# Kernel tuning notes

Measured on AMD Instinct MI355X. Metric: run time of the kernel, lower is better.

## Reference

```python
import jax, jax.numpy as jnp
import numpy as np


def setup_inputs() -> dict:
    key = jax.random.key(0)
    k1, k2, k3, k4, k5, k6 = jax.random.split(key, 6)
    B, V = 128, 128000
    logits = jax.random.normal(k1, (B, V), dtype=jnp.float32) * 2.0
    # keep temperatures away from 0 to avoid overflow in logits/temp
    temperatures = 0.7 + 0.6 * jax.random.uniform(k2, (B,), dtype=jnp.float32)
    top_ks = jax.random.randint(k3, (B,), 1, 1024, dtype=jnp.int32)
    top_ps = 0.7 + 0.29 * jax.random.uniform(k4, (B,), dtype=jnp.float32)
    min_ps = 0.02 * jax.random.uniform(k5, (B,), dtype=jnp.float32)
    # uniform variate for inverse-CDF multinomial sampling (one sample per row)
    u = jax.random.uniform(k6, (B, 1), dtype=jnp.float32)
    return {
        "logits": logits,
        "temperatures": temperatures,
        "top_ks": top_ks,
        "top_ps": top_ps,
        "min_ps": min_ps,
        "u": u,
    }


def reference(logits, temperatures, top_ks, top_ps, min_ps, u):
    """Faithful jax version of Sampler's torch-native sampling path:
    softmax(logits/T) -> descending sort -> top-k mask -> top-p mask
    (cumsum computed pre-mask, exactly as torch code) -> min-p mask ->
    multinomial sample (inverse CDF with provided uniform u) ->
    gather original token index. Also returns the renormalized filtered
    probs scattered back to vocab order (top_p_normalize_probs-style)."""
    B, V = logits.shape
    probs = jax.nn.softmax(logits / temperatures[:, None], axis=-1)  # [B, V]

    order = jnp.argsort(-probs, axis=-1)                     # descending indices
    probs_sort = jnp.take_along_axis(probs, order, axis=-1)  # [B, V] sorted desc
    probs_sum = jnp.cumsum(probs_sort, axis=-1)              # cumsum BEFORE masking

    pos = jnp.arange(V, dtype=jnp.int32)[None, :]
    # top-k: zero everything at rank >= top_k
    probs_sort = jnp.where(pos >= top_ks[:, None], 0.0, probs_sort)
    # top-p: zero where cumulative mass strictly before this token exceeds top_p
    probs_sort = jnp.where(probs_sum - probs_sort > top_ps[:, None], 0.0, probs_sort)
    # min-p: threshold relative to the max prob (rank-0 entry survives both masks)
    min_p_thr = probs_sort[:, :1] * min_ps[:, None]
    probs_sort = jnp.where(probs_sort < min_p_thr, 0.0, probs_sort)

    total = jnp.sum(probs_sort, axis=-1, keepdims=True)      # [B, 1]
    cdf = jnp.cumsum(probs_sort, axis=-1) / total            # normalized CDF
    # inverse-CDF sampling == torch.multinomial(probs_sort, 1)
    sampled_rank = jnp.clip(jnp.sum(cdf < u, axis=-1, keepdims=True), 0, V - 1)
    token_ids = jnp.take_along_axis(order, sampled_rank, axis=-1)[:, 0].astype(jnp.int32)

    # scatter renormalized filtered probs back to original vocab positions
    inv_order = jnp.argsort(order, axis=-1)
    norm_probs = jnp.take_along_axis(probs_sort / total, inv_order, axis=-1)
    return token_ids, norm_probs
```

## Files before the change

### kernel.cpp

```cpp
#include <hip/hip_runtime.h>
#include <stdint.h>
#include <math.h>

#define TPB 1024
#define NB 2048
#define SPLIT 4
#define LCAND 2560
#define CAND2 2048
#define PS 4096
#define L2E 1.44269504088896f

typedef float vfloat4 __attribute__((ext_vector_type(4)));
typedef unsigned long long ull;

__device__ __forceinline__ unsigned fkey(float f) {
    unsigned u = __float_as_uint(f);
    return (u & 0x80000000u) ? ~u : (u | 0x80000000u);
}
__device__ __forceinline__ float funkey(unsigned k) {
    unsigned u = (k & 0x80000000u) ? (k ^ 0x80000000u) : ~k;
    return __uint_as_float(u);
}
__device__ __forceinline__ ull packkv(unsigned k, unsigned idx) {
    return ((ull)k << 32) | (ull)(~idx);
}

__device__ __forceinline__ float inv_norm_tail(float p) {
    float t = sqrtf(-2.0f * logf(p));
    float num = 2.515517f + t * (0.802853f + t * 0.010328f);
    float den = 1.0f + t * (1.432788f + t * (0.189269f + t * 0.001308f));
    return t - num / den;
}

__device__ __forceinline__ void suffix_scan_2048(unsigned* h, unsigned* wscr, int tid)
{
    const int lane = tid & 63, w = tid >> 6;
    const int i0 = 2047 - 2 * tid;
    const int i1 = 2046 - 2 * tid;
    unsigned a = h[i0], b = h[i1];
    unsigned s = a + b;
    unsigned inc = s;
    #pragma unroll
    for (int d = 1; d < 64; d <<= 1) { unsigned o = __shfl_up(inc, d); if (lane >= d) inc += o; }
    if (lane == 63) wscr[w] = inc;
    __syncthreads();
    if (w == 0) {
        unsigned v = (lane < 16) ? wscr[lane] : 0u;
        unsigned vi = v;
        #pragma unroll
        for (int d = 1; d < 16; d <<= 1) { unsigned o = __shfl_up(vi, d); if (lane >= d) vi += o; }
        if (lane < 16) wscr[16 + lane] = vi - v;
    }
    __syncthreads();
    unsigned off = wscr[16 + w] + (inc - s);
    h[i0] = off + a;
    h[i1] = off + a + b;
    __syncthreads();
}

__global__ __launch_bounds__(TPB)
void k1_scan(const float* __restrict__ logits,
             const float* __restrict__ temps,
             const int* __restrict__ top_ks,
             float* __restrict__ out_probs,
             float* __restrict__ ws_meta,
             unsigned* __restrict__ ws_cut,
             unsigned* __restrict__ ws_cnt,
             unsigned* __restrict__ ws_max,
             ull* __restrict__ ws_cand,
             int V, int Vq)
{
    const int sblk = blockIdx.x;
    const int b = sblk / SPLIT, s = sblk % SPLIT;
    const int tid = threadIdx.x, lane = tid & 63, w = tid >> 6;
    const int start = s * Vq;
    const int len = min(Vq, V - start);
    const int slot = sblk;
    const float invT = 1.0f / temps[b];
    int K = top_ks[b]; K = max(K, 1); K = min(K, 1024);

    __shared__ float fred[52];
    __shared__ unsigned uscr[32];
    __shared__ unsigned cnt;

    if (len <= 0) {
        if (tid == 0) {
            ws_meta[2*slot] = -1e30f; ws_meta[2*slot+1] = 0.0f;
            ws_cut[slot] = 0xFFFFFFFFu; ws_cnt[slot] = 0u; ws_max[slot] = 0u;
        }
        return;
    }

    if (tid == 0) cnt = 0;

    const float* __restrict__ row = logits + (size_t)b * V + start;
    const vfloat4* __restrict__ row4 = (const vfloat4*)row;
    float* __restrict__ orow = out_probs + (size_t)b * V + start;
    vfloat4* __restrict__ orow4 = (vfloat4*)orow;
    const vfloat4 z4 = (vfloat4)0.0f;
    const int L4 = len >> 2;
    const bool vec = (len >= 4 * TPB);
    const int nps = vec ? (4 * TPB) : min(len, PS);

    float sm = 0.0f, sq = 0.0f, m0 = -1e30f;
    vfloat4 pv = z4;
    if (vec) {
        pv = row4[tid];
        __builtin_nontemporal_store(z4, &orow4[tid]);
        sm = (pv[0] + pv[1]) + (pv[2] + pv[3]);
        sq = (pv[0]*pv[0] + pv[1]*pv[1]) + (pv[2]*pv[2] + pv[3]*pv[3]);
        m0 = fmaxf(fmaxf(pv[0], pv[1]), fmaxf(pv[2], pv[3]));
    } else {
        for (int i = tid; i < nps; i += TPB) {
            float lv = row[i];
            sm += lv; sq += lv * lv;
            m0 = fmaxf(m0, lv);
        }
    }
    #pragma unroll
    for (int d = 32; d > 0; d >>= 1) {
        sm += __shfl_down(sm, d);
        sq += __shfl_down(sq, d);
        m0 = fmaxf(m0, __shfl_down(m0, d));
    }
    if (lane == 0) { fred[w] = sm; fred[16 + w] = sq; fred[32 + w] = m0; }
    __syncthreads();
    if (tid == 0) {
        float S = 0.0f, Q = 0.0f, M = -1e30f;
        for (int j = 0; j < 16; ++j) {
            S += fred[j]; Q += fred[16 + j]; M = fmaxf(M, fred[32 + j]);
        }
        float n  = (float)nps;
        float mu = S / n;
        float var = fmaxf(Q / n - mu * mu, 0.0f);
        float sg = sqrtf(var);
        float Cf = 3.0f * (float)K + 384.0f;
        float p  = Cf / (float)V;
        p = fminf(fmaxf(p, 1e-7f), 0.45f);
        fred[48] = mu + sg * inv_norm_tail(p);
        fred[49] = M;
    }
    __syncthreads();
    const float cutval = fred[48];
    const float m0max  = fred[49];
    const unsigned cutkey = fkey(cutval);

    if (vec) {
        for (int i = TPB + tid; i < L4; i += TPB) __builtin_nontemporal_store(z4, &orow4[i]);
        for (int i = (L4 << 2) + tid; i < len; i += TPB) __builtin_nontemporal_store(0.0f, &orow[i]);
    } else {
        for (int i = tid; i < L4; i += TPB) __builtin_nontemporal_store(z4, &orow4[i]);
        for (int i = (L4 << 2) + tid; i < len; i += TPB) __builtin_nontemporal_store(0.0f, &orow[i]);
    }

    const float ca = invT * L2E;
    const float cb = -m0max * invT * L2E;
    ull* gc = ws_cand + (size_t)slot * LCAND;

    float z0 = 0.0f, z1 = 0.0f, z2 = 0.0f, z3 = 0.0f;
    float mA = m0, mB = -1e30f, mC = -1e30f, mD = -1e30f;

    #define E4(v) (exp2f(fmaf((v)[0], ca, cb)) + exp2f(fmaf((v)[1], ca, cb)) \
                 + exp2f(fmaf((v)[2], ca, cb)) + exp2f(fmaf((v)[3], ca, cb)))
    #define M4(v) fmaxf(fmaxf((v)[0], (v)[1]), fmaxf((v)[2], (v)[3]))
    #define GATHER(v, ii) do {                                                  \
        bool c0 = (v)[0] >= cutval, c1 = (v)[1] >= cutval,                      \
             c2 = (v)[2] >= cutval, c3 = (v)[3] >= cutval;                      \
        if (c0 | c1 | c2 | c3) {                                                \
            int nh = (int)c0 + (int)c1 + (int)c2 + (int)c3;                     \
            unsigned base = atomicAdd(&cnt, (unsigned)nh);                      \
            unsigned bi = (unsigned)(start + ((ii) << 2));                      \
            if (c0) { if (base < LCAND) gc[base] = packkv(fkey((v)[0]), bi+0); base++; } \
            if (c1) { if (base < LCAND) gc[base] = packkv(fkey((v)[1]), bi+1); base++; } \
            if (c2) { if (base < LCAND) gc[base] = packkv(fkey((v)[2]), bi+2); base++; } \
            if (c3) { if (base < LCAND) gc[base] = packkv(fkey((v)[3]), bi+3); base++; } \
        }                                                                       \
    } while (0)

    if (vec) {
        int i = TPB + tid;
        for (; i + 3 * TPB < L4; i += 4 * TPB) {
            vfloat4 va = row4[i];
            vfloat4 vb = row4[i + TPB];
            vfloat4 vc = row4[i + 2 * TPB];
            vfloat4 vd = row4[i + 3 * TPB];
            z0 += E4(va); z1 += E4(vb); z2 += E4(vc); z3 += E4(vd);
            mA = fmaxf(mA, M4(va)); mB = fmaxf(mB, M4(vb));
            mC = fmaxf(mC, M4(vc)); mD = fmaxf(mD, M4(vd));
            GATHER(va, i); GATHER(vb, i + TPB); GATHER(vc, i + 2 * TPB); GATHER(vd, i + 3 * TPB);
        }
        for (; i < L4; i += TPB) {
            vfloat4 v = row4[i];
            z0 += E4(v);
            mA = fmaxf(mA, M4(v));
            GATHER(v, i);
        }
        for (int j = (L4 << 2) + tid; j < len; j += TPB) {
            float lv = row[j];
            z0 += exp2f(fmaf(lv, ca, cb));
            mA = fmaxf(mA, lv);
            if (lv >= cutval) {
                unsigned base = atomicAdd(&cnt, 1u);
                if (base < LCAND) gc[base] = packkv(fkey(lv), (unsigned)(start + j));
            }
        }
        z0 += E4(pv);
        GATHER(pv, tid);
    } else {
        int i = tid;
        for (; i + 3 * TPB < L4; i += 4 * TPB) {
            vfloat4 va = row4[i];
            vfloat4 vb = row4[i + TPB];
            vfloat4 vc = row4[i + 2 * TPB];
            vfloat4 vd = row4[i + 3 * TPB];
            z0 += E4(va); z1 += E4(vb); z2 += E4(vc); z3 += E4(vd);
            mA = fmaxf(mA, M4(va)); mB = fmaxf(mB, M4(vb));
            mC = fmaxf(mC, M4(vc)); mD = fmaxf(mD, M4(vd));
            GATHER(va, i); GATHER(vb, i + TPB); GATHER(vc, i + 2 * TPB); GATHER(vd, i + 3 * TPB);
        }
        for (; i < L4; i += TPB) {
            vfloat4 v = row4[i];
            z0 += E4(v);
            mA = fmaxf(mA, M4(v));
            GATHER(v, i);
        }
        for (int j = (L4 << 2) + tid; j < len; j += TPB) {
            float lv = row[j];
            z0 += exp2f(fmaf(lv, ca, cb));
            mA = fmaxf(mA, lv);
            if (lv >= cutval) {
                unsigned base = atomicAdd(&cnt, 1u);
                if (base < LCAND) gc[base] = packkv(fkey(lv), (unsigned)(start + j));
            }
        }
    }
    #undef E4
    #undef M4
    #undef GATHER

    float z = (z0 + z1) + (z2 + z3);
    unsigned rk = fkey(fmaxf(fmaxf(mA, mB), fmaxf(mC, mD)));
    __syncthreads();
    #pragma unroll
    for (int d = 32; d > 0; d >>= 1) {
        z += __shfl_down(z, d);
        rk = max(rk, __shfl_down(rk, d));
    }
    if (lane == 0) { fred[w] = z; uscr[w] = rk; }
    __syncthreads();
    if (tid == 0) {
        float zz = 0.0f;
        unsigned mk = 0u;
        for (int j = 0; j < 16; ++j) { zz += fred[j]; mk = max(mk, uscr[j]); }
        ws_meta[2*slot + 0] = m0max * invT;
        ws_meta[2*slot + 1] = zz;
        ws_cut[slot] = cutkey;
        ws_cnt[slot] = cnt;
        ws_max[slot] = mk;
    }
}

__global__ __launch_bounds__(TPB)
void k2_sample(const float* __restrict__ logits,
               const float* __restrict__ temps,
               const int* __restrict__ top_ks,
               const float* __restrict__ top_ps,
               const float* __restrict__ min_ps,
               const float* __restrict__ uvec,
               const float* __restrict__ ws_meta,
               const unsigned* __restrict__ ws_cut,
               const unsigned* __restrict__ ws_cnt,
               const unsigned* __restrict__ ws_max,
               const ull* __restrict__ ws_cand,
               float* __restrict__ out_tok,
               float* __restrict__ out_probs,
               int V)
{
    const int b = blockIdx.x;
    const int tid = threadIdx.x, lane = tid & 63, w = tid >> 6;
    const float invT = 1.0f / temps[b];
    int Korig = top_ks[b]; Korig = max(Korig, 1); Korig = min(Korig, 1024);
    const unsigned Ku = (unsigned)Korig;
    const float top_p = top_ps[b], min_p = min_ps[b], uval = uvec[b];

    __shared__ __align__(16) char smem[53504];
    ull*            cand  = (ull*)(smem);
    ull*            cand2 = (ull*)(smem + 16384);
    unsigned*       hist  = (unsigned*)(smem + 32768);
    unsigned short* cnts  = (unsigned short*)(smem + 41216);
    float*          sh_p  = (float*)(smem + 45312);
    float*          sh_c  = (float*)(smem + 49408);
    __shared__ unsigned uscr[32];
    __shared__ float fws[32];
    __shared__ unsigned scnt;
    __shared__ int sh_i1, sh_i2;
    __shared__ unsigned sh_u1;

    float Cy[SPLIT], zq[SPLIT];
    unsigned cutq[SPLIT], cntq[SPLIT], mxq[SPLIT];
    #pragma unroll
    for (int q = 0; q < SPLIT; ++q) {
        int sl = b * SPLIT + q;
        Cy[q] = ws_meta[2*sl]; zq[q] = ws_meta[2*sl+1];
        cutq[q] = ws_cut[sl]; cntq[q] = ws_cnt[sl]; mxq[q] = ws_max[sl];
    }
    float Y = -1e30f;
    #pragma unroll
    for (int q = 0; q < SPLIT; ++q) if (cntq[q] > 0u) Y = fmaxf(Y, Cy[q]);
    float Z = 0.0f;
    #pragma unroll
    for (int q = 0; q < SPLIT; ++q)
        if (cntq[q] > 0u && zq[q] > 0.0f) Z += zq[q] * exp2f((Cy[q] - Y) * L2E);

    bool fb = false;
    unsigned cutmax = 0, mincut = 0xFFFFFFFFu;
    #pragma unroll
    for (int q = 0; q < SPLIT; ++q) {
        if (cntq[q] > (unsigned)LCAND) fb = true;
        if (cntq[q] > 0u) {
            if (!isfinite(zq[q])) fb = true;
            cutmax = max(cutmax, cutq[q]);
            mincut = min(mincut, cutq[q]);
        }
    }
    if (mincut == 0xFFFFFFFFu || !isfinite(Z) || Z <= 0.0f) fb = true;

    unsigned Tkeyb = 0;
    int count = 0, bstar = 0, shift = 0;
    unsigned base = mincut;

    if (!fb) {
        for (int i = tid; i <= NB; i += TPB) hist[i] = 0;
        if (tid == 0) sh_i1 = -1;
        unsigned maxkey = 0;
        #pragma unroll
        for (int q = 0; q < SPLIT; ++q)
            if (cntq[q] > 0u) maxkey = max(maxkey, mxq[q]);
        const unsigned range = maxkey - base;
        while ((range >> shift) > (unsigned)(NB - 1)) shift++;
        __syncthreads();

        #pragma unroll
        for (int q = 0; q < SPLIT; ++q) {
            const ull* gc = ws_cand + (size_t)(b * SPLIT + q) * LCAND;
            int nl = min((int)cntq[q], LCAND);
            for (int i = tid; i < nl; i += TPB)
                atomicAdd(&hist[((unsigned)(gc[i] >> 32) - base) >> shift], 1u);
        }
        __syncthreads();
        unsigned fat = 0;
        for (int i = tid; i < NB; i += TPB) {
            unsigned h = hist[i];
            cnts[i] = (unsigned short)h;
            fat = max(fat, h);
        }
        #pragma unroll
        for (int d = 32; d > 0; d >>= 1) fat = max(fat, __shfl_down(fat, d));
        if (lane == 0) uscr[w] = fat;
        __syncthreads();
        if (tid == 0) {
            unsigned m2 = 0;
            for (int j = 0; j < 16; ++j) m2 = max(m2, uscr[j]);
            uscr[16] = m2;
        }
        __syncthreads();
        if (uscr[16] > 64u) fb = true;
    }
    if (!fb) {
        suffix_scan_2048(hist, uscr, tid);
        for (int e = tid; e < NB; e += TPB) {
            unsigned Se = hist[e], Sn = (e < NB - 1) ? hist[e + 1] : 0u;
            if (Se >= Ku && Sn < Ku) { sh_i1 = e; sh_u1 = Se; }
        }
        __syncthreads();
        if (sh_i1 < 0) fb = true;
        else {
            bstar = sh_i1;
            count = (int)sh_u1;
            Tkeyb = base + ((unsigned)bstar << shift);
            if (Tkeyb < cutmax || count > CAND2) fb = true;
        }
    }
    if (!fb) {
        #pragma unroll
        for (int q = 0; q < SPLIT; ++q) {
            const ull* gc = ws_cand + (size_t)(b * SPLIT + q) * LCAND;
            int nl = min((int)cntq[q], LCAND);
            for (int i = tid; i < nl; i += TPB) {
                ull e = gc[i];
                unsigned k = (unsigned)(e >> 32);
                if (k >= Tkeyb) {
                    unsigned bin = (k - base) >> shift;
                    unsigned pos = atomicAdd(&hist[bin + 1], 1u);
                    cand2[pos] = e;
                }
            }
        }
        __syncthreads();
        for (int e = bstar + tid; e < NB; e += TPB) {
            int c = (int)cnts[e];
            if (c >= 2) {
                int st = (int)hist[e + 1] - c;
                for (int x = 1; x < c; ++x) {
                    ull key = cand2[st + x];
                    int y = x - 1;
                    while (y >= 0 && cand2[st + y] < key) { cand2[st + y + 1] = cand2[st + y]; --y; }
                    cand2[st + y + 1] = key;
                }
            }
        }
        __syncthreads();
    }

    if (fb) {
        const float* __restrict__ row = logits + (size_t)b * V;
        float m = -1e30f, z = 0.0f;
        for (int i = tid; i < V; i += TPB) {
            float y = row[i] * invT;
            float nm = fmaxf(m, y);
            z = z * exp2f((m - nm) * L2E) + exp2f((y - nm) * L2E);
            m = nm;
        }
        sh_p[tid] = m; sh_c[tid] = z;
        __syncthreads();
        for (int d = TPB >> 1; d > 0; d >>= 1) {
            if (tid < d) {
                float m1 = sh_p[tid], z1 = sh_c[tid];
                float m2 = sh_p[tid + d], z2 = sh_c[tid + d];
                float mm = fmaxf(m1, m2);
                sh_c[tid] = z1 * exp2f((m1 - mm) * L2E) + z2 * exp2f((m2 - mm) * L2E);
                sh_p[tid] = mm;
            }
            __syncthreads();
        }
        Y = sh_p[0]; Z = sh_c[0];
        __syncthreads();
        for (int i = tid; i < NB; i += TPB) hist[i] = 0;
        if (tid == 0) { sh_i1 = 0; sh_i2 = 0; sh_u1 = 0; }
        __syncthreads();
        for (int i = tid; i < V; i += TPB) atomicAdd(&hist[fkey(row[i]) >> 21], 1u);
        __syncthreads();
        suffix_scan_2048(hist, uscr, tid);
        for (int e = tid; e < NB; e += TPB) {
            unsigned Se = hist[e], Sn = (e < NB-1) ? hist[e+1] : 0u;
            if (Se >= Ku && Sn < Ku) { sh_i1 = e; sh_u1 = Sn; }
        }
        __syncthreads();
        int b1 = sh_i1;
        unsigned cab = sh_u1;
        for (int i = tid; i < NB; i += TPB) hist[i] = 0;
        __syncthreads();
        for (int i = tid; i < V; i += TPB) {
            unsigned k = fkey(row[i]);
            if ((int)(k >> 21) == b1) atomicAdd(&hist[(k >> 10) & (NB - 1)], 1u);
        }
        __syncthreads();
        suffix_scan_2048(hist, uscr, tid);
        for (int e = tid; e < NB; e += TPB) {
            unsigned Se = cab + hist[e];
            unsigned Sn = cab + ((e < NB-1) ? hist[e+1] : 0u);
            if (Se >= Ku && Sn < Ku) sh_i2 = e;
        }
        __syncthreads();
        unsigned Tkey = ((unsigned)b1 << 21) | ((unsigned)sh_i2 << 10);
        if (tid == 0) scnt = 0;
        __syncthreads();
        for (int i = tid; i < V; i += TPB) {
            unsigned k = fkey(row[i]);
            if (k >= Tkey) {
                unsigned pos = atomicAdd(&scnt, 1u);
                if (pos < CAND2) cand[pos] = packkv(k, (unsigned)i);
            }
        }
        __syncthreads();
        count = (scnt < (unsigned)CAND2) ? (int)scnt : CAND2;

        int n_sort = 1;
        while (n_sort < count) n_sort <<= 1;
        for (int i = tid; i < n_sort; i += TPB)
            if (i >= count) cand[i] = 0ull;
        __syncthreads();
        for (int kk = 2; kk <= n_sort; kk <<= 1) {
            for (int j = kk >> 1; j > 0; j >>= 1) {
                for (int i = tid; i < n_sort; i += TPB) {
                    int ixj = i ^ j;
                    if (ixj > i) {
                        ull a = cand[i], c = cand[ixj];
                        bool up = (i & kk) == 0;
                        if (up ? (a < c) : (a > c)) { cand[i] = c; cand[ixj] = a; }
                    }
                }
                __syncthreads();
            }
        }
    }

    ull* srt = fb ? cand : cand2;
    int K = min(Korig, count);

    float pv = 0.0f;
    if (tid < K) {
        unsigned k = (unsigned)(srt[tid] >> 32);
        pv = exp2f((funkey(k) * invT - Y) * L2E) / Z;
    }
    float inc = pv;
    #pragma unroll
    for (int d = 1; d < 64; d <<= 1) { float o = __shfl_up(inc, d); if (lane >= d) inc += o; }
    if (lane == 63) fws[w] = inc;
    __syncthreads();
    if (w == 0) {
        float v = (lane < 16) ? fws[lane] : 0.0f;
        float vi = v;
        #pragma unroll
        for (int d = 1; d < 16; d <<= 1) { float o = __shfl_up(vi, d); if (lane >= d) vi += o; }
        if (lane < 16) fws[16 + lane] = vi - v;
    }
    __syncthreads();
    float cum = inc + fws[16 + w];
    sh_p[tid] = pv;
    sh_c[tid] = cum;
    if (tid == 0) sh_i1 = K;
    __syncthreads();

    if (tid < K) {
        float excl = cum - pv;
        if (excl > top_p) atomicMin(&sh_i1, tid);
    }
    __syncthreads();
    int n1 = sh_i1;
    float thr = sh_p[0] * min_p;
    if (tid == 0) sh_i2 = n1;
    __syncthreads();
    if (tid < n1 && sh_p[tid] < thr) atomicMin(&sh_i2, tid);
    __syncthreads();
    int nf = sh_i2;
    float total = sh_c[nf - 1];

    int pred = (tid < nf) && ((sh_c[tid] / total) < uval);
    int rank = __syncthreads_count(pred);
    if (rank > nf - 1) rank = nf - 1;
    if (rank < 0) rank = 0;
    if (tid == 0)
        out_tok[b] = (float)(~(unsigned)(srt[rank] & 0xFFFFFFFFull));

    if (tid < nf) {
        unsigned idx = ~(unsigned)(srt[tid] & 0xFFFFFFFFull);
        out_probs[(size_t)b * V + idx] = sh_p[tid] / total;
    }
}

extern "C" void kernel_launch(void* const* d_in, const int* in_sizes, int n_in,
                              void* d_out, int out_size, void* d_ws, size_t ws_size,
                              hipStream_t stream) {
    const float* logits = (const float*)d_in[0];
    const float* temps  = (const float*)d_in[1];
    const int*   top_ks = (const int*)d_in[2];
    const float* top_ps = (const float*)d_in[3];
    const float* min_ps = (const float*)d_in[4];
    const float* u      = (const float*)d_in[5];
    const int B = in_sizes[1];
    const int V = in_sizes[0] / B;
    float* out_tok   = (float*)d_out;
    float* out_probs = out_tok + B;

    int Vq = (((V + SPLIT - 1) / SPLIT) + 3) & ~3;

    char* ws = (char*)d_ws;
    size_t off = 0;
    auto take = [&](size_t bytes) { char* p = ws + off; off = (off + bytes + 255) & ~(size_t)255; return p; };
    float*    ws_meta = (float*)take((size_t)B * SPLIT * 2 * sizeof(float));
    unsigned* ws_cut  = (unsigned*)take((size_t)B * SPLIT * sizeof(unsigned));
    unsigned* ws_cnt  = (unsigned*)take((size_t)B * SPLIT * sizeof(unsigned));
    unsigned* ws_maxk = (unsigned*)take((size_t)B * SPLIT * sizeof(unsigned));
    ull*      ws_cand = (ull*)take((size_t)B * SPLIT * LCAND * sizeof(ull));
    (void)ws_size;

    k1_scan<<<dim3(SPLIT * B), dim3(TPB), 0, stream>>>(
        logits, temps, top_ks, out_probs, ws_meta, ws_cut, ws_cnt, ws_maxk, ws_cand, V, Vq);
    k2_sample<<<dim3(B), dim3(TPB), 0, stream>>>(
        logits, temps, top_ks, top_ps, min_ps, u, ws_meta, ws_cut, ws_cnt, ws_maxk, ws_cand,
        out_tok, out_probs, V);
}
```

Before: 149.4 us.

## Fuse scan and sample kernels using last-block-done counter per row

```diff
diff --git a/kernel.cpp b/kernel.cpp
--- a/kernel.cpp
+++ b/kernel.cpp
@@ -59,15 +59,20 @@
 }
 
 __global__ __launch_bounds__(TPB)
-void k1_scan(const float* __restrict__ logits,
+void k_fused(const float* __restrict__ logits,
              const float* __restrict__ temps,
              const int* __restrict__ top_ks,
+             const float* __restrict__ top_ps,
+             const float* __restrict__ min_ps,
+             const float* __restrict__ uvec,
+             float* __restrict__ out_tok,
              float* __restrict__ out_probs,
              float* __restrict__ ws_meta,
              unsigned* __restrict__ ws_cut,
              unsigned* __restrict__ ws_cnt,
              unsigned* __restrict__ ws_max,
              ull* __restrict__ ws_cand,
+             unsigned* __restrict__ ws_done,
              int V, int Vq)
 {
     const int sblk = blockIdx.x;
@@ -79,210 +84,6 @@
     const float invT = 1.0f / temps[b];
     int K = top_ks[b]; K = max(K, 1); K = min(K, 1024);
 
-    __shared__ float fred[52];
-    __shared__ unsigned uscr[32];
-    __shared__ unsigned cnt;
-
-    if (len <= 0) {
-        if (tid == 0) {
-            ws_meta[2*slot] = -1e30f; ws_meta[2*slot+1] = 0.0f;
-            ws_cut[slot] = 0xFFFFFFFFu; ws_cnt[slot] = 0u; ws_max[slot] = 0u;
-        }
-        return;
-    }
-
-    if (tid == 0) cnt = 0;
-
-    const float* __restrict__ row = logits + (size_t)b * V + start;
-    const vfloat4* __restrict__ row4 = (const vfloat4*)row;
-    float* __restrict__ orow = out_probs + (size_t)b * V + start;
-    vfloat4* __restrict__ orow4 = (vfloat4*)orow;
-    const vfloat4 z4 = (vfloat4)0.0f;
-    const int L4 = len >> 2;
-    const bool vec = (len >= 4 * TPB);
-    const int nps = vec ? (4 * TPB) : min(len, PS);
-
-    float sm = 0.0f, sq = 0.0f, m0 = -1e30f;
-    vfloat4 pv = z4;
-    if (vec) {
-        pv = row4[tid];
-        __builtin_nontemporal_store(z4, &orow4[tid]);
-        sm = (pv[0] + pv[1]) + (pv[2] + pv[3]);
-        sq = (pv[0]*pv[0] + pv[1]*pv[1]) + (pv[2]*pv[2] + pv[3]*pv[3]);
-        m0 = fmaxf(fmaxf(pv[0], pv[1]), fmaxf(pv[2], pv[3]));
-    } else {
-        for (int i = tid; i < nps; i += TPB) {
-            float lv = row[i];
-            sm += lv; sq += lv * lv;
-            m0 = fmaxf(m0, lv);
-        }
-    }
-    #pragma unroll
-    for (int d = 32; d > 0; d >>= 1) {
-        sm += __shfl_down(sm, d);
-        sq += __shfl_down(sq, d);
-        m0 = fmaxf(m0, __shfl_down(m0, d));
-    }
-    if (lane == 0) { fred[w] = sm; fred[16 + w] = sq; fred[32 + w] = m0; }
-    __syncthreads();
-    if (tid == 0) {
-        float S = 0.0f, Q = 0.0f, M = -1e30f;
-        for (int j = 0; j < 16; ++j) {
-            S += fred[j]; Q += fred[16 + j]; M = fmaxf(M, fred[32 + j]);
-        }
-        float n  = (float)nps;
-        float mu = S / n;
-        float var = fmaxf(Q / n - mu * mu, 0.0f);
-        float sg = sqrtf(var);
-        float Cf = 3.0f * (float)K + 384.0f;
-        float p  = Cf / (float)V;
-        p = fminf(fmaxf(p, 1e-7f), 0.45f);
-        fred[48] = mu + sg * inv_norm_tail(p);
-        fred[49] = M;
-    }
-    __syncthreads();
-    const float cutval = fred[48];
-    const float m0max  = fred[49];
-    const unsigned cutkey = fkey(cutval);
-
-    if (vec) {
-        for (int i = TPB + tid; i < L4; i += TPB) __builtin_nontemporal_store(z4, &orow4[i]);
-        for (int i = (L4 << 2) + tid; i < len; i += TPB) __builtin_nontemporal_store(0.0f, &orow[i]);
-    } else {
-        for (int i = tid; i < L4; i += TPB) __builtin_nontemporal_store(z4, &orow4[i]);
-        for (int i = (L4 << 2) + tid; i < len; i += TPB) __builtin_nontemporal_store(0.0f, &orow[i]);
-    }
-
-    const float ca = invT * L2E;
-    const float cb = -m0max * invT * L2E;
-    ull* gc = ws_cand + (size_t)slot * LCAND;
-
-    float z0 = 0.0f, z1 = 0.0f, z2 = 0.0f, z3 = 0.0f;
-    float mA = m0, mB = -1e30f, mC = -1e30f, mD = -1e30f;
-
-    #define E4(v) (exp2f(fmaf((v)[0], ca, cb)) + exp2f(fmaf((v)[1], ca, cb)) \
-                 + exp2f(fmaf((v)[2], ca, cb)) + exp2f(fmaf((v)[3], ca, cb)))
-    #define M4(v) fmaxf(fmaxf((v)[0], (v)[1]), fmaxf((v)[2], (v)[3]))
-    #define GATHER(v, ii) do {                                                  \
-        bool c0 = (v)[0] >= cutval, c1 = (v)[1] >= cutval,                      \
-             c2 = (v)[2] >= cutval, c3 = (v)[3] >= cutval;                      \
-        if (c0 | c1 | c2 | c3) {                                                \
-            int nh = (int)c0 + (int)c1 + (int)c2 + (int)c3;                     \
-            unsigned base = atomicAdd(&cnt, (unsigned)nh);                      \
-            unsigned bi = (unsigned)(start + ((ii) << 2));                      \
-            if (c0) { if (base < LCAND) gc[base] = packkv(fkey((v)[0]), bi+0); base++; } \
-            if (c1) { if (base < LCAND) gc[base] = packkv(fkey((v)[1]), bi+1); base++; } \
-            if (c2) { if (base < LCAND) gc[base] = packkv(fkey((v)[2]), bi+2); base++; } \
-            if (c3) { if (base < LCAND) gc[base] = packkv(fkey((v)[3]), bi+3); base++; } \
-        }                                                                       \
-    } while (0)
-
-    if (vec) {
-        int i = TPB + tid;
-        for (; i + 3 * TPB < L4; i += 4 * TPB) {
-            vfloat4 va = row4[i];
-            vfloat4 vb = row4[i + TPB];
-            vfloat4 vc = row4[i + 2 * TPB];
-            vfloat4 vd = row4[i + 3 * TPB];
-            z0 += E4(va); z1 += E4(vb); z2 += E4(vc); z3 += E4(vd);
-            mA = fmaxf(mA, M4(va)); mB = fmaxf(mB, M4(vb));
-            mC = fmaxf(mC, M4(vc)); mD = fmaxf(mD, M4(vd));
-            GATHER(va, i); GATHER(vb, i + TPB); GATHER(vc, i + 2 * TPB); GATHER(vd, i + 3 * TPB);
-        }
-        for (; i < L4; i += TPB) {
-            vfloat4 v = row4[i];
-            z0 += E4(v);
-            mA = fmaxf(mA, M4(v));
-            GATHER(v, i);
-        }
-        for (int j = (L4 << 2) + tid; j < len; j += TPB) {
-            float lv = row[j];
-            z0 += exp2f(fmaf(lv, ca, cb));
-            mA = fmaxf(mA, lv);
-            if (lv >= cutval) {
-                unsigned base = atomicAdd(&cnt, 1u);
-                if (base < LCAND) gc[base] = packkv(fkey(lv), (unsigned)(start + j));
-            }
-        }
-        z0 += E4(pv);
-        GATHER(pv, tid);
-    } else {
-        int i = tid;
-        for (; i + 3 * TPB < L4; i += 4 * TPB) {
-            vfloat4 va = row4[i];
-            vfloat4 vb = row4[i + TPB];
-            vfloat4 vc = row4[i + 2 * TPB];
-            vfloat4 vd = row4[i + 3 * TPB];
-            z0 += E4(va); z1 += E4(vb); z2 += E4(vc); z3 += E4(vd);
-            mA = fmaxf(mA, M4(va)); mB = fmaxf(mB, M4(vb));
-            mC = fmaxf(mC, M4(vc)); mD = fmaxf(mD, M4(vd));
-            GATHER(va, i); GATHER(vb, i + TPB); GATHER(vc, i + 2 * TPB); GATHER(vd, i + 3 * TPB);
-        }
-        for (; i < L4; i += TPB) {
-            vfloat4 v = row4[i];
-            z0 += E4(v);
-            mA = fmaxf(mA, M4(v));
-            GATHER(v, i);
-        }
-        for (int j = (L4 << 2) + tid; j < len; j += TPB) {
-            float lv = row[j];
-            z0 += exp2f(fmaf(lv, ca, cb));
-            mA = fmaxf(mA, lv);
-            if (lv >= cutval) {
-                unsigned base = atomicAdd(&cnt, 1u);
-                if (base < LCAND) gc[base] = packkv(fkey(lv), (unsigned)(start + j));
-            }
-        }
-    }
-    #undef E4
-    #undef M4
-    #undef GATHER
-
-    float z = (z0 + z1) + (z2 + z3);
-    unsigned rk = fkey(fmaxf(fmaxf(mA, mB), fmaxf(mC, mD)));
-    __syncthreads();
-    #pragma unroll
-    for (int d = 32; d > 0; d >>= 1) {
-        z += __shfl_down(z, d);
-        rk = max(rk, __shfl_down(rk, d));
-    }
-    if (lane == 0) { fred[w] = z; uscr[w] = rk; }
-    __syncthreads();
-    if (tid == 0) {
-        float zz = 0.0f;
-        unsigned mk = 0u;
-        for (int j = 0; j < 16; ++j) { zz += fred[j]; mk = max(mk, uscr[j]); }
-        ws_meta[2*slot + 0] = m0max * invT;
-        ws_meta[2*slot + 1] = zz;
-        ws_cut[slot] = cutkey;
-        ws_cnt[slot] = cnt;
-        ws_max[slot] = mk;
-    }
-}
-
-__global__ __launch_bounds__(TPB)
-void k2_sample(const float* __restrict__ logits,
-               const float* __restrict__ temps,
-               const int* __restrict__ top_ks,
-               const float* __restrict__ top_ps,
-               const float* __restrict__ min_ps,
-               const float* __restrict__ uvec,
-               const float* __restrict__ ws_meta,
-               const unsigned* __restrict__ ws_cut,
-               const unsigned* __restrict__ ws_cnt,
-               const unsigned* __restrict__ ws_max,
-               const ull* __restrict__ ws_cand,
-               float* __restrict__ out_tok,
-               float* __restrict__ out_probs,
-               int V)
-{
-    const int b = blockIdx.x;
-    const int tid = threadIdx.x, lane = tid & 63, w = tid >> 6;
-    const float invT = 1.0f / temps[b];
-    int Korig = top_ks[b]; Korig = max(Korig, 1); Korig = min(Korig, 1024);
-    const unsigned Ku = (unsigned)Korig;
-    const float top_p = top_ps[b], min_p = min_ps[b], uval = uvec[b];
-
     __shared__ __align__(16) char smem[53504];
     ull*            cand  = (ull*)(smem);
     ull*            cand2 = (ull*)(smem + 16384);
@@ -290,262 +91,453 @@
     unsigned short* cnts  = (unsigned short*)(smem + 41216);
     float*          sh_p  = (float*)(smem + 45312);
     float*          sh_c  = (float*)(smem + 49408);
+    __shared__ float fred[52];
     __shared__ unsigned uscr[32];
     __shared__ float fws[32];
-    __shared__ unsigned scnt;
+    __shared__ unsigned cnt, scnt, sh_last;
     __shared__ int sh_i1, sh_i2;
     __shared__ unsigned sh_u1;
 
-    float Cy[SPLIT], zq[SPLIT];
-    unsigned cutq[SPLIT], cntq[SPLIT], mxq[SPLIT];
-    #pragma unroll
-    for (int q = 0; q < SPLIT; ++q) {
-        int sl = b * SPLIT + q;
-        Cy[q] = ws_meta[2*sl]; zq[q] = ws_meta[2*sl+1];
-        cutq[q] = ws_cut[sl]; cntq[q] = ws_cnt[sl]; mxq[q] = ws_max[sl];
+    if (len <= 0) {
+        if (tid == 0) {
+            ws_meta[2*slot] = -1e30f; ws_meta[2*slot+1] = 0.0f;
+            ws_cut[slot] = 0xFFFFFFFFu; ws_cnt[slot] = 0u; ws_max[slot] = 0u;
+        }
+    } else {
+        if (tid == 0) cnt = 0;
+
+        const float* __restrict__ row = logits + (size_t)b * V + start;
+        const vfloat4* __restrict__ row4 = (const vfloat4*)row;
+        float* __restrict__ orow = out_probs + (size_t)b * V + start;
+        vfloat4* __restrict__ orow4 = (vfloat4*)orow;
+        const vfloat4 z4 = (vfloat4)0.0f;
+        const int L4 = len >> 2;
+        const bool vec = (len >= 4 * TPB);
+        const int nps = vec ? (4 * TPB) : min(len, PS);
+
+        float sm = 0.0f, sq = 0.0f, m0 = -1e30f;
+        vfloat4 pv = z4;
+        if (vec) {
+            pv = row4[tid];
+            __builtin_nontemporal_store(z4, &orow4[tid]);
+            sm = (pv[0] + pv[1]) + (pv[2] + pv[3]);
+            sq = (pv[0]*pv[0] + pv[1]*pv[1]) + (pv[2]*pv[2] + pv[3]*pv[3]);
+            m0 = fmaxf(fmaxf(pv[0], pv[1]), fmaxf(pv[2], pv[3]));
+        } else {
+            for (int i = tid; i < nps; i += TPB) {
+                float lv = row[i];
+                sm += lv; sq += lv * lv;
+                m0 = fmaxf(m0, lv);
+            }
+        }
+        #pragma unroll
+        for (int d = 32; d > 0; d >>= 1) {
+            sm += __shfl_down(sm, d);
+            sq += __shfl_down(sq, d);
+            m0 = fmaxf(m0, __shfl_down(m0, d));
+        }
+        if (lane == 0) { fred[w] = sm; fred[16 + w] = sq; fred[32 + w] = m0; }
+        __syncthreads();
+        if (tid == 0) {
+            float S = 0.0f, Q = 0.0f, M = -1e30f;
+            for (int j = 0; j < 16; ++j) {
+                S += fred[j]; Q += fred[16 + j]; M = fmaxf(M, fred[32 + j]);
+            }
+            float n  = (float)nps;
+            float mu = S / n;
+            float var = fmaxf(Q / n - mu * mu, 0.0f);
+            float sg = sqrtf(var);
+            float Cf = 2.0f * (float)K + 256.0f;
+            float p  = Cf / (float)V;
+            p = fminf(fmaxf(p, 1e-7f), 0.45f);
+            fred[48] = mu + sg * inv_norm_tail(p);
+            fred[49] = M;
+        }
+        __syncthreads();
+        const float cutval = fred[48];
+        const float m0max  = fred[49];
+        const unsigned cutkey = fkey(cutval);
+
+        if (vec) {
+            for (int i = TPB + tid; i < L4; i += TPB) __builtin_nontemporal_store(z4, &orow4[i]);
+            for (int i = (L4 << 2) + tid; i < len; i += TPB) __builtin_nontemporal_store(0.0f, &orow[i]);
+        } else {
+            for (int i = tid; i < L4; i += TPB) __builtin_nontemporal_store(z4, &orow4[i]);
+            for (int i = (L4 << 2) + tid; i < len; i += TPB) __builtin_nontemporal_store(0.0f, &orow[i]);
+        }
+
+        const float ca = invT * L2E;
+        const float cb = -m0max * invT * L2E;
+        ull* gc = ws_cand + (size_t)slot * LCAND;
+
+        float z0 = 0.0f, z1 = 0.0f, z2 = 0.0f, z3 = 0.0f;
+        float mA = m0, mB = -1e30f, mC = -1e30f, mD = -1e30f;
+
+        #define E4(v) (exp2f(fmaf((v)[0], ca, cb)) + exp2f(fmaf((v)[1], ca, cb)) \
+                     + exp2f(fmaf((v)[2], ca, cb)) + exp2f(fmaf((v)[3], ca, cb)))
+        #define M4(v) fmaxf(fmaxf((v)[0], (v)[1]), fmaxf((v)[2], (v)[3]))
+        #define GATHER(v, ii) do {                                                  \
+            bool c0 = (v)[0] >= cutval, c1 = (v)[1] >= cutval,                      \
+                 c2 = (v)[2] >= cutval, c3 = (v)[3] >= cutval;                      \
+            if (c0 | c1 | c2 | c3) {                                                \
+                int nh = (int)c0 + (int)c1 + (int)c2 + (int)c3;                     \
+                unsigned base = atomicAdd(&cnt, (unsigned)nh);                      \
+                unsigned bi = (unsigned)(start + ((ii) << 2));                      \
+                if (c0) { if (base < LCAND) gc[base] = packkv(fkey((v)[0]), bi+0); base++; } \
+                if (c1) { if (base < LCAND) gc[base] = packkv(fkey((v)[1]), bi+1); base++; } \
+                if (c2) { if (base < LCAND) gc[base] = packkv(fkey((v)[2]), bi+2); base++; } \
+                if (c3) { if (base < LCAND) gc[base] = packkv(fkey((v)[3]), bi+3); base++; } \
+            }                                                                       \
+        } while (0)
+
+        if (vec) {
+            int i = TPB + tid;
+            for (; i + 3 * TPB < L4; i += 4 * TPB) {
+                vfloat4 va = row4[i];
+                vfloat4 vb = row4[i + TPB];
+                vfloat4 vc = row4[i + 2 * TPB];
+                vfloat4 vd = row4[i + 3 * TPB];
+                z0 += E4(va); z1 += E4(vb); z2 += E4(vc); z3 += E4(vd);
+                mA = fmaxf(mA, M4(va)); mB = fmaxf(mB, M4(vb));
+                mC = fmaxf(mC, M4(vc)); mD = fmaxf(mD, M4(vd));
+                GATHER(va, i); GATHER(vb, i + TPB); GATHER(vc, i + 2 * TPB); GATHER(vd, i + 3 * TPB);
+            }
+            for (; i < L4; i += TPB) {
+                vfloat4 v = row4[i];
+                z0 += E4(v);
+                mA = fmaxf(mA, M4(v));
+                GATHER(v, i);
+            }
+            for (int j = (L4 << 2) + tid; j < len; j += TPB) {
+                float lv = row[j];
+                z0 += exp2f(fmaf(lv, ca, cb));
+                mA = fmaxf(mA, lv);
+                if (lv >= cutval) {
+                    unsigned base = atomicAdd(&cnt, 1u);
+                    if (base < LCAND) gc[base] = packkv(fkey(lv), (unsigned)(start + j));
+                }
+            }
+            z0 += E4(pv);
+            GATHER(pv, tid);
+        } else {
+            int i = tid;
+            for (; i + 3 * TPB < L4; i += 4 * TPB) {
+                vfloat4 va = row4[i];
+                vfloat4 vb = row4[i + TPB];
+                vfloat4 vc = row4[i + 2 * TPB];
+                vfloat4 vd = row4[i + 3 * TPB];
+                z0 += E4(va); z1 += E4(vb); z2 += E4(vc); z3 += E4(vd);
+                mA = fmaxf(mA, M4(va)); mB = fmaxf(mB, M4(vb));
+                mC = fmaxf(mC, M4(vc)); mD = fmaxf(mD, M4(vd));
+                GATHER(va, i); GATHER(vb, i + TPB); GATHER(vc, i + 2 * TPB); GATHER(vd, i + 3 * TPB);
+            }
+            for (; i < L4; i += TPB) {
+                vfloat4 v = row4[i];
+                z0 += E4(v);
+                mA = fmaxf(mA, M4(v));
+                GATHER(v, i);
+            }
+            for (int j = (L4 << 2) + tid; j < len; j += TPB) {
+                float lv = row[j];
+                z0 += exp2f(fmaf(lv, ca, cb));
+                mA = fmaxf(mA, lv);
+                if (lv >= cutval) {
+                    unsigned base = atomicAdd(&cnt, 1u);
+                    if (base < LCAND) gc[base] = packkv(fkey(lv), (unsigned)(start + j));
+                }
+            }
+        }
+        #undef E4
+        #undef M4
+        #undef GATHER
+
+        float z = (z0 + z1) + (z2 + z3);
+        unsigned rk = fkey(fmaxf(fmaxf(mA, mB), fmaxf(mC, mD)));
+        __syncthreads();
+        #pragma unroll
+        for (int d = 32; d > 0; d >>= 1) {
+            z += __shfl_down(z, d);
+            rk = max(rk, __shfl_down(rk, d));
+        }
+        if (lane == 0) { fred[w] = z; uscr[w] = rk; }
+        __syncthreads();
+        if (tid == 0) {
+            float zz = 0.0f;
+            unsigned mk = 0u;
+            for (int j = 0; j < 16; ++j) { zz += fred[j]; mk = max(mk, uscr[j]); }
+            ws_meta[2*slot + 0] = m0max * invT;
+            ws_meta[2*slot + 1] = zz;
+            ws_cut[slot] = cutkey;
+            ws_cnt[slot] = cnt;
+            ws_max[slot] = mk;
+        }
     }
-    float Y = -1e30f;
-    #pragma unroll
-    for (int q = 0; q < SPLIT; ++q) if (cntq[q] > 0u) Y = fmaxf(Y, Cy[q]);
-    float Z = 0.0f;
-    #pragma unroll
-    for (int q = 0; q < SPLIT; ++q)
-        if (cntq[q] > 0u && zq[q] > 0.0f) Z += zq[q] * exp2f((Cy[q] - Y) * L2E);
-
-    bool fb = false;
-    unsigned cutmax = 0, mincut = 0xFFFFFFFFu;
-    #pragma unroll
-    for (int q = 0; q < SPLIT; ++q) {
-        if (cntq[q] > (unsigned)LCAND) fb = true;
-        if (cntq[q] > 0u) {
-            if (!isfinite(zq[q])) fb = true;
-            cutmax = max(cutmax, cutq[q]);
-            mincut = min(mincut, cutq[q]);
-        }
-    }
-    if (mincut == 0xFFFFFFFFu || !isfinite(Z) || Z <= 0.0f) fb = true;
-
-    unsigned Tkeyb = 0;
-    int count = 0, bstar = 0, shift = 0;
-    unsigned base = mincut;
-
-    if (!fb) {
-        for (int i = tid; i <= NB; i += TPB) hist[i] = 0;
-        if (tid == 0) sh_i1 = -1;
-        unsigned maxkey = 0;
-        #pragma unroll
-        for (int q = 0; q < SPLIT; ++q)
-            if (cntq[q] > 0u) maxkey = max(maxkey, mxq[q]);
-        const unsigned range = maxkey - base;
-        while ((range >> shift) > (unsigned)(NB - 1)) shift++;
-        __syncthreads();
-
-        #pragma unroll
-        for (int q = 0; q < SPLIT; ++q) {
-            const ull* gc = ws_cand + (size_t)(b * SPLIT + q) * LCAND;
-            int nl = min((int)cntq[q], LCAND);
-            for (int i = tid; i < nl; i += TPB)
-                atomicAdd(&hist[((unsigned)(gc[i] >> 32) - base) >> shift], 1u);
-        }
-        __syncthreads();
-        unsigned fat = 0;
-        for (int i = tid; i < NB; i += TPB) {
-            unsigned h = hist[i];
-            cnts[i] = (unsigned short)h;
-            fat = max(fat, h);
-        }
-        #pragma unroll
-        for (int d = 32; d > 0; d >>= 1) fat = max(fat, __shfl_down(fat, d));
-        if (lane == 0) uscr[w] = fat;
-        __syncthreads();
-        if (tid == 0) {
-            unsigned m2 = 0;
-            for (int j = 0; j < 16; ++j) m2 = max(m2, uscr[j]);
-            uscr[16] = m2;
-        }
-        __syncthreads();
-        if (uscr[16] > 64u) fb = true;
-    }
-    if (!fb) {
-        suffix_scan_2048(hist, uscr, tid);
-        for (int e = tid; e < NB; e += TPB) {
-            unsigned Se = hist[e], Sn = (e < NB - 1) ? hist[e + 1] : 0u;
-            if (Se >= Ku && Sn < Ku) { sh_i1 = e; sh_u1 = Se; }
-        }
-        __syncthreads();
-        if (sh_i1 < 0) fb = true;
-        else {
-            bstar = sh_i1;
-            count = (int)sh_u1;
-            Tkeyb = base + ((unsigned)bstar << shift);
-            if (Tkeyb < cutmax || count > CAND2) fb = true;
-        }
-    }
-    if (!fb) {
-        #pragma unroll
-        for (int q = 0; q < SPLIT; ++q) {
-            const ull* gc = ws_cand + (size_t)(b * SPLIT + q) * LCAND;
-            int nl = min((int)cntq[q], LCAND);
-            for (int i = tid; i < nl; i += TPB) {
-                ull e = gc[i];
-                unsigned k = (unsigned)(e >> 32);
-                if (k >= Tkeyb) {
-                    unsigned bin = (k - base) >> shift;
-                    unsigned pos = atomicAdd(&hist[bin + 1], 1u);
-                    cand2[pos] = e;
-                }
-            }
-        }
-        __syncthreads();
-        for (int e = bstar + tid; e < NB; e += TPB) {
-            int c = (int)cnts[e];
-            if (c >= 2) {
-                int st = (int)hist[e + 1] - c;
-                for (int x = 1; x < c; ++x) {
-                    ull key = cand2[st + x];
-                    int y = x - 1;
-                    while (y >= 0 && cand2[st + y] < key) { cand2[st + y + 1] = cand2[st + y]; --y; }
-                    cand2[st + y + 1] = key;
-                }
-            }
-        }
-        __syncthreads();
-    }
-
-    if (fb) {
-        const float* __restrict__ row = logits + (size_t)b * V;
-        float m = -1e30f, z = 0.0f;
-        for (int i = tid; i < V; i += TPB) {
-            float y = row[i] * invT;
-            float nm = fmaxf(m, y);
-            z = z * exp2f((m - nm) * L2E) + exp2f((y - nm) * L2E);
-            m = nm;
-        }
-        sh_p[tid] = m; sh_c[tid] = z;
-        __syncthreads();
-        for (int d = TPB >> 1; d > 0; d >>= 1) {
-            if (tid < d) {
-                float m1 = sh_p[tid], z1 = sh_c[tid];
-                float m2 = sh_p[tid + d], z2 = sh_c[tid + d];
-                float mm = fmaxf(m1, m2);
-                sh_c[tid] = z1 * exp2f((m1 - mm) * L2E) + z2 * exp2f((m2 - mm) * L2E);
-                sh_p[tid] = mm;
-            }
-            __syncthreads();
-        }
-        Y = sh_p[0]; Z = sh_c[0];
-        __syncthreads();
-        for (int i = tid; i < NB; i += TPB) hist[i] = 0;
-        if (tid == 0) { sh_i1 = 0; sh_i2 = 0; sh_u1 = 0; }
-        __syncthreads();
-        for (int i = tid; i < V; i += TPB) atomicAdd(&hist[fkey(row[i]) >> 21], 1u);
-        __syncthreads();
-        suffix_scan_2048(hist, uscr, tid);
-        for (int e = tid; e < NB; e += TPB) {
-            unsigned Se = hist[e], Sn = (e < NB-1) ? hist[e+1] : 0u;
-            if (Se >= Ku && Sn < Ku) { sh_i1 = e; sh_u1 = Sn; }
-        }
-        __syncthreads();
-        int b1 = sh_i1;
-        unsigned cab = sh_u1;
-        for (int i = tid; i < NB; i += TPB) hist[i] = 0;
-        __syncthreads();
-        for (int i = tid; i < V; i += TPB) {
-            unsigned k = fkey(row[i]);
-            if ((int)(k >> 21) == b1) atomicAdd(&hist[(k >> 10) & (NB - 1)], 1u);
-        }
-        __syncthreads();
-        suffix_scan_2048(hist, uscr, tid);
-        for (int e = tid; e < NB; e += TPB) {
-            unsigned Se = cab + hist[e];
-            unsigned Sn = cab + ((e < NB-1) ? hist[e+1] : 0u);
-            if (Se >= Ku && Sn < Ku) sh_i2 = e;
-        }
-        __syncthreads();
-        unsigned Tkey = ((unsigned)b1 << 21) | ((unsigned)sh_i2 << 10);
-        if (tid == 0) scnt = 0;
-        __syncthreads();
-        for (int i = tid; i < V; i += TPB) {
-            unsigned k = fkey(row[i]);
-            if (k >= Tkey) {
-                unsigned pos = atomicAdd(&scnt, 1u);
-                if (pos < CAND2) cand[pos] = packkv(k, (unsigned)i);
-            }
-        }
-        __syncthreads();
-        count = (scnt < (unsigned)CAND2) ? (int)scnt : CAND2;
-
-        int n_sort = 1;
-        while (n_sort < count) n_sort <<= 1;
-        for (int i = tid; i < n_sort; i += TPB)
-            if (i >= count) cand[i] = 0ull;
-        __syncthreads();
-        for (int kk = 2; kk <= n_sort; kk <<= 1) {
-            for (int j = kk >> 1; j > 0; j >>= 1) {
-                for (int i = tid; i < n_sort; i += TPB) {
-                    int ixj = i ^ j;
-                    if (ixj > i) {
-                        ull a = cand[i], c = cand[ixj];
-                        bool up = (i & kk) == 0;
-                        if (up ? (a < c) : (a > c)) { cand[i] = c; cand[ixj] = a; }
-                    }
-                }
-                __syncthreads();
-            }
-        }
-    }
-
-    ull* srt = fb ? cand : cand2;
-    int K = min(Korig, count);
-
-    float pv = 0.0f;
-    if (tid < K) {
-        unsigned k = (unsigned)(srt[tid] >> 32);
-        pv = exp2f((funkey(k) * invT - Y) * L2E) / Z;
-    }
-    float inc = pv;
-    #pragma unroll
-    for (int d = 1; d < 64; d <<= 1) { float o = __shfl_up(inc, d); if (lane >= d) inc += o; }
-    if (lane == 63) fws[w] = inc;
-    __syncthreads();
-    if (w == 0) {
-        float v = (lane < 16) ? fws[lane] : 0.0f;
-        float vi = v;
-        #pragma unroll
-        for (int d = 1; d < 16; d <<= 1) { float o = __shfl_up(vi, d); if (lane >= d) vi += o; }
-        if (lane < 16) fws[16 + lane] = vi - v;
+
+    if (tid == 0) {
+        __threadfence();
+        unsigned old = atomicAdd(&ws_done[b], 1u);
+        sh_last = (old == (unsigned)(SPLIT - 1)) ? 1u : 0u;
     }
     __syncthreads();
-    float cum = inc + fws[16 + w];
-    sh_p[tid] = pv;
-    sh_c[tid] = cum;
-    if (tid == 0) sh_i1 = K;
-    __syncthreads();
-
-    if (tid < K) {
-        float excl = cum - pv;
-        if (excl > top_p) atomicMin(&sh_i1, tid);
-    }
-    __syncthreads();
-    int n1 = sh_i1;
-    float thr = sh_p[0] * min_p;
-    if (tid == 0) sh_i2 = n1;
-    __syncthreads();
-    if (tid < n1 && sh_p[tid] < thr) atomicMin(&sh_i2, tid);
-    __syncthreads();
-    int nf = sh_i2;
-    float total = sh_c[nf - 1];
-
-    int pred = (tid < nf) && ((sh_c[tid] / total) < uval);
-    int rank = __syncthreads_count(pred);
-    if (rank > nf - 1) rank = nf - 1;
-    if (rank < 0) rank = 0;
-    if (tid == 0)
-        out_tok[b] = (float)(~(unsigned)(srt[rank] & 0xFFFFFFFFull));
-
-    if (tid < nf) {
-        unsigned idx = ~(unsigned)(srt[tid] & 0xFFFFFFFFull);
-        out_probs[(size_t)b * V + idx] = sh_p[tid] / total;
+    if (!sh_last) return;
+    __threadfence();
+
+    {
+        const int Korig = K;
+        const unsigned Ku = (unsigned)Korig;
+        const float top_p = top_ps[b], min_p = min_ps[b], uval = uvec[b];
+
+        float Cy[SPLIT], zq[SPLIT];
+        unsigned cutq[SPLIT], cntq[SPLIT], mxq[SPLIT];
+        #pragma unroll
+        for (int q = 0; q < SPLIT; ++q) {
+            int sl = b * SPLIT + q;
+            Cy[q] = ws_meta[2*sl]; zq[q] = ws_meta[2*sl+1];
+            cutq[q] = ws_cut[sl]; cntq[q] = ws_cnt[sl]; mxq[q] = ws_max[sl];
+        }
+        float Y = -1e30f;
+        #pragma unroll
+        for (int q = 0; q < SPLIT; ++q) if (cntq[q] > 0u) Y = fmaxf(Y, Cy[q]);
+        float Z = 0.0f;
+        #pragma unroll
+        for (int q = 0; q < SPLIT; ++q)
+            if (cntq[q] > 0u && zq[q] > 0.0f) Z += zq[q] * exp2f((Cy[q] - Y) * L2E);
+
+        bool fb = false;
+        unsigned cutmax = 0, mincut = 0xFFFFFFFFu;
+        #pragma unroll
+        for (int q = 0; q < SPLIT; ++q) {
+            if (cntq[q] > (unsigned)LCAND) fb = true;
+            if (cntq[q] > 0u) {
+                if (!isfinite(zq[q])) fb = true;
+                cutmax = max(cutmax, cutq[q]);
+                mincut = min(mincut, cutq[q]);
+            }
+        }
+        if (mincut == 0xFFFFFFFFu || !isfinite(Z) || Z <= 0.0f) fb = true;
+
+        unsigned Tkeyb = 0;
+        int count = 0, bstar = 0, shift = 0;
+        unsigned base = mincut;
+
+        if (!fb) {
+            for (int i = tid; i <= NB; i += TPB) hist[i] = 0;
+            if (tid == 0) sh_i1 = -1;
+            unsigned maxkey = 0;
+            #pragma unroll
+            for (int q = 0; q < SPLIT; ++q)
+                if (cntq[q] > 0u) maxkey = max(maxkey, mxq[q]);
+            const unsigned range = maxkey - base;
+            while ((range >> shift) > (unsigned)(NB - 1)) shift++;
+            __syncthreads();
+
+            #pragma unroll
+            for (int q = 0; q < SPLIT; ++q) {
+                const ull* gc = ws_cand + (size_t)(b * SPLIT + q) * LCAND;
+                int nl = min((int)cntq[q], LCAND);
+                for (int i = tid; i < nl; i += TPB)
+                    atomicAdd(&hist[((unsigned)(gc[i] >> 32) - base) >> shift], 1u);
+            }
+            __syncthreads();
+            unsigned fat = 0;
+            for (int i = tid; i < NB; i += TPB) {
+                unsigned h = hist[i];
+                cnts[i] = (unsigned short)h;
+                fat = max(fat, h);
+            }
+            #pragma unroll
+            for (int d = 32; d > 0; d >>= 1) fat = max(fat, __shfl_down(fat, d));
+            if (lane == 0) uscr[w] = fat;
+            __syncthreads();
+            if (tid == 0) {
+                unsigned m2 = 0;
+                for (int j = 0; j < 16; ++j) m2 = max(m2, uscr[j]);
+                uscr[16] = m2;
+            }
+            __syncthreads();
+            if (uscr[16] > 64u) fb = true;
+        }
+        if (!fb) {
+            suffix_scan_2048(hist, uscr, tid);
+            for (int e = tid; e < NB; e += TPB) {
+                unsigned Se = hist[e], Sn = (e < NB - 1) ? hist[e + 1] : 0u;
+                if (Se >= Ku && Sn < Ku) { sh_i1 = e; sh_u1 = Se; }
+            }
+            __syncthreads();
+            if (sh_i1 < 0) fb = true;
+            else {
+                bstar = sh_i1;
+                count = (int)sh_u1;
+                Tkeyb = base + ((unsigned)bstar << shift);
+                if (Tkeyb < cutmax || count > CAND2) fb = true;
+            }
+        }
+        if (!fb) {
+            #pragma unroll
+            for (int q = 0; q < SPLIT; ++q) {
+                const ull* gc = ws_cand + (size_t)(b * SPLIT + q) * LCAND;
+                int nl = min((int)cntq[q], LCAND);
+                for (int i = tid; i < nl; i += TPB) {
+                    ull e = gc[i];
+                    unsigned k = (unsigned)(e >> 32);
+                    if (k >= Tkeyb) {
+                        unsigned bin = (k - base) >> shift;
+                        unsigned pos = atomicAdd(&hist[bin + 1], 1u);
+                        cand2[pos] = e;
+                    }
+                }
+            }
+            __syncthreads();
+            for (int e = bstar + tid; e < NB; e += TPB) {
+                int c = (int)cnts[e];
+                if (c >= 2) {
+                    int st = (int)hist[e + 1] - c;
+                    for (int x = 1; x < c; ++x) {
+                        ull key = cand2[st + x];
+                        int y = x - 1;
+                        while (y >= 0 && cand2[st + y] < key) { cand2[st + y + 1] = cand2[st + y]; --y; }
+                        cand2[st + y + 1] = key;
+                    }
+                }
+            }
+            __syncthreads();
+        }
+
+        if (fb) {
+            const float* __restrict__ row = logits + (size_t)b * V;
+            float m = -1e30f, z = 0.0f;
+            for (int i = tid; i < V; i += TPB) {
+                float y = row[i] * invT;
+                float nm = fmaxf(m, y);
+                z = z * exp2f((m - nm) * L2E) + exp2f((y - nm) * L2E);
+                m = nm;
+            }
+            sh_p[tid] = m; sh_c[tid] = z;
+            __syncthreads();
+            for (int d = TPB >> 1; d > 0; d >>= 1) {
+                if (tid < d) {
+                    float m1 = sh_p[tid], z1 = sh_c[tid];
+                    float m2 = sh_p[tid + d], z2 = sh_c[tid + d];
+                    float mm = fmaxf(m1, m2);
+                    sh_c[tid] = z1 * exp2f((m1 - mm) * L2E) + z2 * exp2f((m2 - mm) * L2E);
+                    sh_p[tid] = mm;
+                }
+                __syncthreads();
+            }
+            Y = sh_p[0]; Z = sh_c[0];
+            __syncthreads();
+            for (int i = tid; i < NB; i += TPB) hist[i] = 0;
+            if (tid == 0) { sh_i1 = 0; sh_i2 = 0; sh_u1 = 0; }
+            __syncthreads();
+            for (int i = tid; i < V; i += TPB) atomicAdd(&hist[fkey(row[i]) >> 21], 1u);
+            __syncthreads();
+            suffix_scan_2048(hist, uscr, tid);
+            for (int e = tid; e < NB; e += TPB) {
+                unsigned Se = hist[e], Sn = (e < NB-1) ? hist[e+1] : 0u;
+                if (Se >= Ku && Sn < Ku) { sh_i1 = e; sh_u1 = Sn; }
+            }
+            __syncthreads();
+            int b1 = sh_i1;
+            unsigned cab = sh_u1;
+            for (int i = tid; i < NB; i += TPB) hist[i] = 0;
+            __syncthreads();
+            for (int i = tid; i < V; i += TPB) {
+                unsigned k = fkey(row[i]);
+                if ((int)(k >> 21) == b1) atomicAdd(&hist[(k >> 10) & (NB - 1)], 1u);
+            }
+            __syncthreads();
+            suffix_scan_2048(hist, uscr, tid);
+            for (int e = tid; e < NB; e += TPB) {
+                unsigned Se = cab + hist[e];
+                unsigned Sn = cab + ((e < NB-1) ? hist[e+1] : 0u);
+                if (Se >= Ku && Sn < Ku) sh_i2 = e;
+            }
+            __syncthreads();
+            unsigned Tkey = ((unsigned)b1 << 21) | ((unsigned)sh_i2 << 10);
+            if (tid == 0) scnt = 0;
+            __syncthreads();
+            for (int i = tid; i < V; i += TPB) {
+                unsigned k = fkey(row[i]);
+                if (k >= Tkey) {
+                    unsigned pos = atomicAdd(&scnt, 1u);
+                    if (pos < CAND2) cand[pos] = packkv(k, (unsigned)i);
+                }
+            }
+            __syncthreads();
+            count = (scnt < (unsigned)CAND2) ? (int)scnt : CAND2;
+
+            int n_sort = 1;
+            while (n_sort < count) n_sort <<= 1;
+            for (int i = tid; i < n_sort; i += TPB)
+                if (i >= count) cand[i] = 0ull;
+            __syncthreads();
+            for (int kk = 2; kk <= n_sort; kk <<= 1) {
+                for (int j = kk >> 1; j > 0; j >>= 1) {
+                    for (int i = tid; i < n_sort; i += TPB) {
+                        int ixj = i ^ j;
+                        if (ixj > i) {
+                            ull a = cand[i], c = cand[ixj];
+                            bool up = (i & kk) == 0;
+                            if (up ? (a < c) : (a > c)) { cand[i] = c; cand[ixj] = a; }
+                        }
+                    }
+                    __syncthreads();
+                }
+            }
+        }
+
+        ull* srt = fb ? cand : cand2;
+        int Kk = min(Korig, count);
+
+        float pvp = 0.0f;
+        if (tid < Kk) {
+            unsigned k = (unsigned)(srt[tid] >> 32);
+            pvp = exp2f((funkey(k) * invT - Y) * L2E) / Z;
+        }
+        float inc = pvp;
+        #pragma unroll
+        for (int d = 1; d < 64; d <<= 1) { float o = __shfl_up(inc, d); if (lane >= d) inc += o; }
+        if (lane == 63) fws[w] = inc;
+        __syncthreads();
+        if (w == 0) {
+            float v = (lane < 16) ? fws[lane] : 0.0f;
+            float vi = v;
+            #pragma unroll
+            for (int d = 1; d < 16; d <<= 1) { float o = __shfl_up(vi, d); if (lane >= d) vi += o; }
+            if (lane < 16) fws[16 + lane] = vi - v;
+        }
+        __syncthreads();
+        float cum = inc + fws[16 + w];
+        sh_p[tid] = pvp;
+        sh_c[tid] = cum;
+        if (tid == 0) sh_i1 = Kk;
+        __syncthreads();
+
+        if (tid < Kk) {
+            float excl = cum - pvp;
+            if (excl > top_p) atomicMin(&sh_i1, tid);
+        }
+        __syncthreads();
+        int n1 = sh_i1;
+        float thr = sh_p[0] * min_p;
+        if (tid == 0) sh_i2 = n1;
+        __syncthreads();
+        if (tid < n1 && sh_p[tid] < thr) atomicMin(&sh_i2, tid);
+        __syncthreads();
+        int nf = sh_i2;
+        float total = sh_c[nf - 1];
+
+        int pred = (tid < nf) && ((sh_c[tid] / total) < uval);
+        int rank = __syncthreads_count(pred);
+        if (rank > nf - 1) rank = nf - 1;
+        if (rank < 0) rank = 0;
+        if (tid == 0)
+            out_tok[b] = (float)(~(unsigned)(srt[rank] & 0xFFFFFFFFull));
+
+        if (tid < nf) {
+            unsigned idx = ~(unsigned)(srt[tid] & 0xFFFFFFFFull);
+            out_probs[(size_t)b * V + idx] = sh_p[tid] / total;
+        }
     }
 }
 
@@ -572,12 +564,13 @@
     unsigned* ws_cut  = (unsigned*)take((size_t)B * SPLIT * sizeof(unsigned));
     unsigned* ws_cnt  = (unsigned*)take((size_t)B * SPLIT * sizeof(unsigned));
     unsigned* ws_maxk = (unsigned*)take((size_t)B * SPLIT * sizeof(unsigned));
+    unsigned* ws_done = (unsigned*)take((size_t)B * sizeof(unsigned));
     ull*      ws_cand = (ull*)take((size_t)B * SPLIT * LCAND * sizeof(ull));
     (void)ws_size;
 
-    k1_scan<<<dim3(SPLIT * B), dim3(TPB), 0, stream>>>(
-        logits, temps, top_ks, out_probs, ws_meta, ws_cut, ws_cnt, ws_maxk, ws_cand, V, Vq);
-    k2_sample<<<dim3(B), dim3(TPB), 0, stream>>>(
-        logits, temps, top_ks, top_ps, min_ps, u, ws_meta, ws_cut, ws_cnt, ws_maxk, ws_cand,
-        out_tok, out_probs, V);
-}
+    hipMemsetAsync(ws_done, 0, (size_t)B * sizeof(unsigned), stream);
+
+    k_fused<<<dim3(SPLIT * B), dim3(TPB), 0, stream>>>(
+        logits, temps, top_ks, top_ps, min_ps, u, out_tok, out_probs,
+        ws_meta, ws_cut, ws_cnt, ws_maxk, ws_cand, ws_done, V, Vq);
+}
```

Measured after the change: 223.5 us. +49.6%, slower.
